# Kernel optimization log

Measured on AMD Instinct MI355X. Metric: run time of the kernel, lower is better.

The kernel has to match this reference:

```python
import jax, jax.numpy as jnp
import numpy as np

B, L, LC, C, H = 4, 1024, 1024, 1024, 16
HD = C // H
SCALE = 0.25 / (HD ** 0.5)
EPS = 1e-5

def _ln(x):
    mu = jnp.mean(x, axis=-1, keepdims=True)
    var = jnp.mean(jnp.square(x - mu), axis=-1, keepdims=True)
    return (x - mu) * jax.lax.rsqrt(var + EPS)

def setup_inputs() -> dict:
    key = jax.random.key(0)
    ks = jax.random.split(key, 16)
    s = 0.02
    return {
        'x': jax.random.normal(ks[0], (B, L, C), jnp.float32),
        'context': jax.random.normal(ks[1], (B, LC, C), jnp.float32),
        'cond_BD': jax.random.normal(ks[2], (B, 1, 6, C), jnp.float32),
        'attn_bias': jax.random.normal(ks[3], (B, H, L, LC), jnp.float32) * 0.1,
        'ada_gss': jax.random.normal(ks[4], (1, 1, 6, C), jnp.float32) / (C ** 0.5),
        'Wq': jax.random.normal(ks[5], (C, C), jnp.float32) * s,
        'Wk': jax.random.normal(ks[6], (C, C), jnp.float32) * s,
        'Wv': jax.random.normal(ks[7], (C, C), jnp.float32) * s,
        'Wo': jax.random.normal(ks[8], (C, C), jnp.float32) * s,
        'bo': jnp.zeros((C,), jnp.float32),
        'W1': jax.random.normal(ks[9], (4 * C, C), jnp.float32) * s,
        'b1': jnp.zeros((4 * C,), jnp.float32),
        'W2': jax.random.normal(ks[10], (C, 4 * C), jnp.float32) * s,
        'b2': jnp.zeros((C,), jnp.float32),
    }

def reference(x, context, cond_BD, attn_bias, ada_gss, Wq, Wk, Wv, Wo, bo, W1, b1, W2, b2):
    # AdaLN params: [B,1,6,C] -> six [B,1,C] tensors
    g = ada_gss + cond_BD
    gamma1, gamma2, scale1, scale2, shift1, shift2 = [g[:, :, i] for i in range(6)]

    # --- cross attention branch ---
    mod_x = _ln(x) * (scale1 + 1.0) + shift1  # [B,L,C]
    q = jnp.einsum('blc,dc->bld', mod_x, Wq).reshape(B, L, H, HD).transpose(0, 2, 1, 3)
    k = jnp.einsum('bmc,dc->bmd', context, Wk).reshape(B, LC, H, HD).transpose(0, 2, 1, 3)
    v = jnp.einsum('bmc,dc->bmd', context, Wv).reshape(B, LC, H, HD).transpose(0, 2, 1, 3)
    attn = jnp.einsum('bhld,bhmd->bhlm', q, k) * SCALE + attn_bias
    attn = jax.nn.softmax(attn, axis=-1)
    out = jnp.einsum('bhlm,bhmd->bhld', attn, v).transpose(0, 2, 1, 3).reshape(B, L, C)
    attn_out = jnp.einsum('blc,dc->bld', out, Wo) + bo
    x = x + attn_out * gamma1

    # --- FFN branch ---
    mod_f = _ln(x) * (scale2 + 1.0) + shift2
    h = jax.nn.gelu(jnp.einsum('blc,hc->blh', mod_f, W1) + b1, approximate=True)
    ffn_out = jnp.einsum('blh,ch->blc', h, W2) + b2
    return x + ffn_out * gamma2
```

## Files before the change

### kernel.cpp

```cpp
#include <hip/hip_runtime.h>

typedef _Float16 half8 __attribute__((ext_vector_type(8)));
typedef _Float16 half4v __attribute__((ext_vector_type(4)));
typedef float f32x4 __attribute__((ext_vector_type(4)));

#define MFMA16(a, b, c) __builtin_amdgcn_mfma_f32_16x16x32_f16((a), (b), (c), 0, 0, 0)

__device__ __forceinline__ void gl2lds16(const void* g, void* l) {
  __builtin_amdgcn_global_load_lds(
      (const __attribute__((address_space(1))) void*)g,
      (__attribute__((address_space(3))) void*)l, 16, 0, 0);
}

__device__ __forceinline__ void cast8(const float* s, _Float16* d, int i) {
  float4 a = *(const float4*)(s + i);
  float4 b = *(const float4*)(s + i + 4);
  half8 o;
  o[0] = (_Float16)a.x; o[1] = (_Float16)a.y; o[2] = (_Float16)a.z; o[3] = (_Float16)a.w;
  o[4] = (_Float16)b.x; o[5] = (_Float16)b.y; o[6] = (_Float16)b.z; o[7] = (_Float16)b.w;
  *(half8*)(d + i) = o;
}

__global__ void cast_all_kernel(const float* s0, const float* s1, const float* s2,
                                const float* s3, const float* s4, const float* s5,
                                const float* s6, _Float16* d0, _Float16* d1,
                                _Float16* d2, _Float16* d3, _Float16* d4,
                                _Float16* d5, _Float16* d6) {
  int b = blockIdx.x;
  const float* s;
  _Float16* d;
  int off;
  if (b < 2048)      { s = s0; d = d0; off = b; }
  else if (b < 2560) { s = s1; d = d1; off = b - 2048; }
  else if (b < 3072) { s = s2; d = d2; off = b - 2560; }
  else if (b < 3584) { s = s3; d = d3; off = b - 3072; }
  else if (b < 4096) { s = s4; d = d4; off = b - 3584; }
  else if (b < 6144) { s = s5; d = d5; off = b - 4096; }
  else               { s = s6; d = d6; off = b - 6144; }
  cast8(s, d, (off * 256 + threadIdx.x) * 8);
}

__global__ void ln_mod_kernel(const float* __restrict__ x, const float* __restrict__ cond,
                              const float* __restrict__ ada, _Float16* __restrict__ out,
                              int sidx, int hidx) {
  int row = blockIdx.x;
  int b = row >> 10;
  int t = threadIdx.x;
  const float* xr = x + (size_t)row * 1024;
  float4 v = *(const float4*)(xr + t * 4);
  float s = v.x + v.y + v.z + v.w;
  float s2 = v.x * v.x + v.y * v.y + v.z * v.z + v.w * v.w;
#pragma unroll
  for (int m = 32; m >= 1; m >>= 1) {
    s += __shfl_xor(s, m, 64);
    s2 += __shfl_xor(s2, m, 64);
  }
  __shared__ float red[8];
  int w = t >> 6;
  if ((t & 63) == 0) { red[w * 2] = s; red[w * 2 + 1] = s2; }
  __syncthreads();
  s = red[0] + red[2] + red[4] + red[6];
  s2 = red[1] + red[3] + red[5] + red[7];
  float mu = s * (1.f / 1024.f);
  float var = s2 * (1.f / 1024.f) - mu * mu;
  float rstd = rsqrtf(var + 1e-5f);
  int c = t * 4;
  float4 sc = *(const float4*)(cond + (size_t)b * 6144 + sidx * 1024 + c);
  float4 sh = *(const float4*)(cond + (size_t)b * 6144 + hidx * 1024 + c);
  float4 sa = *(const float4*)(ada + sidx * 1024 + c);
  float4 ha = *(const float4*)(ada + hidx * 1024 + c);
  half4v o;
  o[0] = (_Float16)((v.x - mu) * rstd * (sc.x + sa.x + 1.f) + sh.x + ha.x);
  o[1] = (_Float16)((v.y - mu) * rstd * (sc.y + sa.y + 1.f) + sh.y + ha.y);
  o[2] = (_Float16)((v.z - mu) * rstd * (sc.z + sa.z + 1.f) + sh.z + ha.z);
  o[3] = (_Float16)((v.w - mu) * rstd * (sc.w + sa.w + 1.f) + sh.w + ha.w);
  *(half4v*)(out + (size_t)row * 1024 + c) = o;
}

template <int EPI>
__global__ __launch_bounds__(256) void gemm_f16(
    const _Float16* __restrict__ A, const _Float16* __restrict__ W,
    int M, int N, int K, void* __restrict__ outp,
    const float* __restrict__ bias, const float* __restrict__ res,
    const float* __restrict__ cond, const float* __restrict__ ada, int gidx) {
  __shared__ __align__(16) _Float16 lA[128 * 32];
  __shared__ __align__(16) _Float16 lB[128 * 32];
  int t = threadIdx.x;
  int lane = t & 63;
  int w = t >> 6;
  int wr = w >> 1, wc = w & 1;
  int l16 = lane & 15, lg = lane >> 4;
  int bm = blockIdx.y * 128, bn = blockIdx.x * 128;
  f32x4 acc[4][4] = {};
  int e0 = t * 8;
  int e1 = 2048 + t * 8;
  int r0 = e0 >> 5, c0 = e0 & 31;
  int r1 = e1 >> 5, c1 = e1 & 31;
  const _Float16* Ab = A + (size_t)bm * K;
  const _Float16* Wb = W + (size_t)bn * K;
  for (int kt = 0; kt < K; kt += 32) {
    gl2lds16(Ab + (size_t)r0 * K + kt + c0, &lA[e0]);
    gl2lds16(Ab + (size_t)r1 * K + kt + c1, &lA[e1]);
    gl2lds16(Wb + (size_t)r0 * K + kt + c0, &lB[e0]);
    gl2lds16(Wb + (size_t)r1 * K + kt + c1, &lB[e1]);
    __syncthreads();
    half8 af[4], bf[4];
#pragma unroll
    for (int m = 0; m < 4; ++m)
      af[m] = *(const half8*)&lA[(wr * 64 + m * 16 + l16) * 32 + lg * 8];
#pragma unroll
    for (int n = 0; n < 4; ++n)
      bf[n] = *(const half8*)&lB[(wc * 64 + n * 16 + l16) * 32 + lg * 8];
#pragma unroll
    for (int m = 0; m < 4; ++m)
#pragma unroll
      for (int n = 0; n < 4; ++n)
        acc[m][n] = MFMA16(af[m], bf[n], acc[m][n]);
    __syncthreads();
  }
#pragma unroll
  for (int m = 0; m < 4; ++m) {
#pragma unroll
    for (int n = 0; n < 4; ++n) {
      int gc = bn + wc * 64 + n * 16 + l16;
      int gr0 = bm + wr * 64 + m * 16 + lg * 4;
#pragma unroll
      for (int r = 0; r < 4; ++r) {
        int gr = gr0 + r;
        float v = acc[m][n][r];
        if constexpr (EPI == 0) {
          int b = gr >> 10, l = gr & 1023, h = gc >> 6, hd = gc & 63;
          ((_Float16*)outp)[(((size_t)(b * 16 + h)) * 1024 + l) * 64 + hd] = (_Float16)v;
        } else if constexpr (EPI == 1) {
          float g = ada[gidx * 1024 + gc] + cond[(size_t)(gr >> 10) * 6144 + gidx * 1024 + gc];
          ((float*)outp)[(size_t)gr * 1024 + gc] =
              res[(size_t)gr * 1024 + gc] + (v + bias[gc]) * g;
        } else {
          float xx = v + bias[gc];
          float u = 0.7978845608028654f * (xx + 0.044715f * xx * xx * xx);
          float e = __expf(2.f * u);
          float th = (e - 1.f) / (e + 1.f);
          ((_Float16*)outp)[(size_t)gr * 4096 + gc] = (_Float16)(0.5f * xx * (1.f + th));
        }
      }
    }
  }
}

__global__ void transpose_v_kernel(const _Float16* __restrict__ v16, _Float16* __restrict__ vt16) {
  int bh = blockIdx.y, ktile = blockIdx.x;
  __shared__ _Float16 tile[64][72];
  int t = threadIdx.x;
  int r = t >> 2, c0 = (t & 3) * 16;
  const _Float16* src = v16 + ((size_t)bh * 1024 + ktile * 64) * 64;
  half8 a = *(const half8*)(src + r * 64 + c0);
  half8 b = *(const half8*)(src + r * 64 + c0 + 8);
#pragma unroll
  for (int j = 0; j < 8; ++j) {
    tile[r][c0 + j] = a[j];
    tile[r][c0 + 8 + j] = b[j];
  }
  __syncthreads();
  half8 oa, ob;
#pragma unroll
  for (int j = 0; j < 8; ++j) {
    oa[j] = tile[c0 + j][r];
    ob[j] = tile[c0 + 8 + j][r];
  }
  _Float16* dst = vt16 + ((size_t)bh * 64 + r) * 1024 + ktile * 64 + c0;
  *(half8*)dst = oa;
  *(half8*)(dst + 8) = ob;
}

__global__ __launch_bounds__(256, 4) void attn_kernel(
    const _Float16* __restrict__ q16, const _Float16* __restrict__ k16,
    const _Float16* __restrict__ vt16, const float* __restrict__ bias,
    _Float16* __restrict__ o16) {
  int bh = blockIdx.y;
  int qb = blockIdx.x;
  int t = threadIdx.x, w = t >> 6, lane = t & 63;
  int l16 = lane & 15, lg = lane >> 4;
  int qRowW = qb * 64 + w * 16;
  const size_t bhoff = (size_t)bh * 65536;
  half8 aq[2];
#pragma unroll
  for (int ks = 0; ks < 2; ++ks)
    aq[ks] = *(const half8*)(q16 + bhoff + (size_t)(qRowW + l16) * 64 + ks * 32 + lg * 8);
  f32x4 oacc[4] = {};
  float mrun = -1e30f, lrun = 0.f;
  __shared__ __align__(16) _Float16 pbuf[4][16][80];
  const float* bb = bias + (size_t)bh * 1048576 + (size_t)(qRowW + l16) * 1024;
  const _Float16* kb = k16 + bhoff;
  const _Float16* vb = vt16 + bhoff;
  f32x4 nb[4];
#pragma unroll
  for (int kk = 0; kk < 4; ++kk) nb[kk] = *(const f32x4*)(bb + kk * 16 + lg * 4);
  for (int kt = 0; kt < 1024; kt += 64) {
    f32x4 s[4] = {};
#pragma unroll
    for (int ks = 0; ks < 2; ++ks) {
#pragma unroll
      for (int kk = 0; kk < 4; ++kk) {
        half8 kf = *(const half8*)(kb + (size_t)(kt + kk * 16 + l16) * 64 + ks * 32 + lg * 8);
        s[kk] = MFMA16(kf, aq[ks], s[kk]);
      }
    }
    float p[4][4];
    float tm = -1e30f;
#pragma unroll
    for (int kk = 0; kk < 4; ++kk)
#pragma unroll
      for (int r = 0; r < 4; ++r) {
        p[kk][r] = s[kk][r] * 0.03125f + nb[kk][r];
        tm = fmaxf(tm, p[kk][r]);
      }
    if (kt < 960) {
#pragma unroll
      for (int kk = 0; kk < 4; ++kk)
        nb[kk] = *(const f32x4*)(bb + kt + 64 + kk * 16 + lg * 4);
    }
    tm = fmaxf(tm, __shfl_xor(tm, 16, 64));
    tm = fmaxf(tm, __shfl_xor(tm, 32, 64));
    int noskip = !__all(tm <= mrun);
    float mnew = noskip ? fmaxf(mrun, tm) : mrun;
    float ts = 0.f;
#pragma unroll
    for (int kk = 0; kk < 4; ++kk)
#pragma unroll
      for (int r = 0; r < 4; ++r) {
        p[kk][r] = exp2f((p[kk][r] - mnew) * 1.442695041f);
        ts += p[kk][r];
      }
    ts += __shfl_xor(ts, 16, 64);
    ts += __shfl_xor(ts, 32, 64);
    if (noskip) {
      float scl = exp2f((mrun - mnew) * 1.442695041f);
      lrun = lrun * scl + ts;
      mrun = mnew;
      float sclr[4];
#pragma unroll
      for (int r = 0; r < 4; ++r) sclr[r] = __shfl(scl, lg * 4 + r, 16);
#pragma unroll
      for (int n = 0; n < 4; ++n)
#pragma unroll
        for (int r = 0; r < 4; ++r) oacc[n][r] *= sclr[r];
    } else {
      lrun += ts;
    }
#pragma unroll
    for (int kk = 0; kk < 4; ++kk) {
      half4v ph;
#pragma unroll
      for (int r = 0; r < 4; ++r) ph[r] = (_Float16)p[kk][r];
      *(half4v*)&pbuf[w][l16][kk * 16 + lg * 4] = ph;
    }
#pragma unroll
    for (int ks = 0; ks < 2; ++ks) {
      half8 ap = *(const half8*)&pbuf[w][l16][ks * 32 + lg * 8];
#pragma unroll
      for (int n = 0; n < 4; ++n) {
        half8 bv = *(const half8*)(vb + (size_t)(n * 16 + l16) * 1024 + kt + ks * 32 + lg * 8);
        oacc[n] = MFMA16(ap, bv, oacc[n]);
      }
    }
  }
  float inv = 1.f / lrun;
  float invr[4];
#pragma unroll
  for (int r = 0; r < 4; ++r) invr[r] = __shfl(inv, lg * 4 + r, 16);
  int b = bh >> 4, h = bh & 15;
#pragma unroll
  for (int r = 0; r < 4; ++r) {
    int row = qRowW + lg * 4 + r;
#pragma unroll
    for (int n = 0; n < 4; ++n)
      o16[((size_t)b * 1024 + row) * 1024 + h * 64 + n * 16 + l16] =
          (_Float16)(oacc[n][r] * invr[r]);
  }
}

extern "C" void kernel_launch(void* const* d_in, const int* in_sizes, int n_in,
                              void* d_out, int out_size, void* d_ws, size_t ws_size,
                              hipStream_t stream) {
  const float* x = (const float*)d_in[0];
  const float* ctx = (const float*)d_in[1];
  const float* cond = (const float*)d_in[2];
  const float* bias = (const float*)d_in[3];
  const float* ada = (const float*)d_in[4];
  const float* Wq = (const float*)d_in[5];
  const float* Wk = (const float*)d_in[6];
  const float* Wv = (const float*)d_in[7];
  const float* Wo = (const float*)d_in[8];
  const float* bo = (const float*)d_in[9];
  const float* W1 = (const float*)d_in[10];
  const float* b1 = (const float*)d_in[11];
  const float* W2 = (const float*)d_in[12];
  const float* b2 = (const float*)d_in[13];

  char* ws = (char*)d_ws;
  const size_t MB = 1u << 20;
  _Float16* wq16 = (_Float16*)(ws + 0 * MB);
  _Float16* wk16 = (_Float16*)(ws + 2 * MB);
  _Float16* wv16 = (_Float16*)(ws + 4 * MB);
  _Float16* wo16 = (_Float16*)(ws + 6 * MB);
  _Float16* w116 = (_Float16*)(ws + 8 * MB);
  _Float16* w216 = (_Float16*)(ws + 16 * MB);
  _Float16* modx = (_Float16*)(ws + 24 * MB);
  _Float16* ctx16 = (_Float16*)(ws + 32 * MB);
  _Float16* q16 = (_Float16*)(ws + 40 * MB);
  _Float16* k16 = (_Float16*)(ws + 48 * MB);
  _Float16* v16 = (_Float16*)(ws + 56 * MB);
  _Float16* vt16 = (_Float16*)(ws + 64 * MB);
  _Float16* h16 = (_Float16*)(ws + 40 * MB);
  _Float16* o16 = (_Float16*)(ws + 72 * MB);
  float* x1 = (float*)(ws + 80 * MB);

  cast_all_kernel<<<8192, 256, 0, stream>>>(ctx, Wq, Wk, Wv, Wo, W1, W2,
                                            ctx16, wq16, wk16, wv16, wo16, w116, w216);

  ln_mod_kernel<<<4096, 256, 0, stream>>>(x, cond, ada, modx, 2, 4);

  dim3 gN1024(8, 32);
  gemm_f16<0><<<gN1024, 256, 0, stream>>>(modx, wq16, 4096, 1024, 1024, q16,
                                          nullptr, nullptr, nullptr, nullptr, 0);
  gemm_f16<0><<<gN1024, 256, 0, stream>>>(ctx16, wk16, 4096, 1024, 1024, k16,
                                          nullptr, nullptr, nullptr, nullptr, 0);
  gemm_f16<0><<<gN1024, 256, 0, stream>>>(ctx16, wv16, 4096, 1024, 1024, v16,
                                          nullptr, nullptr, nullptr, nullptr, 0);

  transpose_v_kernel<<<dim3(16, 64), 256, 0, stream>>>(v16, vt16);

  attn_kernel<<<dim3(16, 64), 256, 0, stream>>>(q16, k16, vt16, bias, o16);

  gemm_f16<1><<<gN1024, 256, 0, stream>>>(o16, wo16, 4096, 1024, 1024, x1,
                                          bo, x, cond, ada, 0);

  ln_mod_kernel<<<4096, 256, 0, stream>>>(x1, cond, ada, modx, 3, 5);

  gemm_f16<2><<<dim3(32, 32), 256, 0, stream>>>(modx, w116, 4096, 4096, 1024, h16,
                                                b1, nullptr, nullptr, nullptr, 0);

  gemm_f16<1><<<gN1024, 256, 0, stream>>>(h16, w216, 4096, 1024, 4096, d_out,
                                          b2, x1, cond, ada, 1);
}
```

Before: 849.5 us.

## Batch QKV GEMMs with transposed V epilogue and split-K attention with LDS bias

Folds the three Q/K/V projection GEMMs into one launch, with a z-dimension selecting the weight, and writes V directly in transposed layout, which removes the separate transpose kernel and its round trip through memory. The attention kernel is restructured so each block handles 16 query rows, with its four waves splitting the key range. Each block stages its 64KB bias tile into LDS with a swizzled async load, and the partial softmax states are merged through LDS at the end. Block IDs are remapped for locality, and the P buffer is XOR-swizzled to avoid bank conflicts. The large LDS footprint lowers occupancy, and the final merge adds extra LDS traffic.

After: 797.7 us. 6.1% less time.

```diff
diff --git a/kernel.cpp b/kernel.cpp
--- a/kernel.cpp
+++ b/kernel.cpp
@@ -75,6 +75,76 @@
   o[2] = (_Float16)((v.z - mu) * rstd * (sc.z + sa.z + 1.f) + sh.z + ha.z);
   o[3] = (_Float16)((v.w - mu) * rstd * (sc.w + sa.w + 1.f) + sh.w + ha.w);
   *(half4v*)(out + (size_t)row * 1024 + c) = o;
+}
+
+__global__ __launch_bounds__(256) void gemm_qkv(
+    const _Float16* __restrict__ modx, const _Float16* __restrict__ ctx16,
+    const _Float16* __restrict__ wq, const _Float16* __restrict__ wk,
+    const _Float16* __restrict__ wv, _Float16* __restrict__ q16,
+    _Float16* __restrict__ k16, _Float16* __restrict__ vt16) {
+  int z = blockIdx.z;
+  const _Float16* A = (z == 0) ? modx : ctx16;
+  const _Float16* W = (z == 0) ? wq : ((z == 1) ? wk : wv);
+  const int K = 1024;
+  __shared__ __align__(16) _Float16 lA[128 * 32];
+  __shared__ __align__(16) _Float16 lB[128 * 32];
+  int t = threadIdx.x;
+  int lane = t & 63;
+  int w = t >> 6;
+  int wr = w >> 1, wc = w & 1;
+  int l16 = lane & 15, lg = lane >> 4;
+  int bm = blockIdx.y * 128, bn = blockIdx.x * 128;
+  f32x4 acc[4][4] = {};
+  int e0 = t * 8;
+  int e1 = 2048 + t * 8;
+  int r0 = e0 >> 5, c0 = e0 & 31;
+  int r1 = e1 >> 5, c1 = e1 & 31;
+  const _Float16* Ab = A + (size_t)bm * K;
+  const _Float16* Wb = W + (size_t)bn * K;
+  for (int kt = 0; kt < K; kt += 32) {
+    gl2lds16(Ab + (size_t)r0 * K + kt + c0, &lA[e0]);
+    gl2lds16(Ab + (size_t)r1 * K + kt + c1, &lA[e1]);
+    gl2lds16(Wb + (size_t)r0 * K + kt + c0, &lB[e0]);
+    gl2lds16(Wb + (size_t)r1 * K + kt + c1, &lB[e1]);
+    __syncthreads();
+    half8 af[4], bf[4];
+#pragma unroll
+    for (int m = 0; m < 4; ++m)
+      af[m] = *(const half8*)&lA[(wr * 64 + m * 16 + l16) * 32 + lg * 8];
+#pragma unroll
+    for (int n = 0; n < 4; ++n)
+      bf[n] = *(const half8*)&lB[(wc * 64 + n * 16 + l16) * 32 + lg * 8];
+#pragma unroll
+    for (int m = 0; m < 4; ++m)
+#pragma unroll
+      for (int n = 0; n < 4; ++n)
+        acc[m][n] = MFMA16(af[m], bf[n], acc[m][n]);
+    __syncthreads();
+  }
+#pragma unroll
+  for (int m = 0; m < 4; ++m) {
+#pragma unroll
+    for (int n = 0; n < 4; ++n) {
+      int gc = bn + wc * 64 + n * 16 + l16;
+      int gr0 = bm + wr * 64 + m * 16 + lg * 4;
+      int h = gc >> 6, hd = gc & 63;
+      if (z < 2) {
+        _Float16* dst = (z == 0) ? q16 : k16;
+#pragma unroll
+        for (int r = 0; r < 4; ++r) {
+          int gr = gr0 + r;
+          int b = gr >> 10, l = gr & 1023;
+          dst[(((size_t)(b * 16 + h)) * 1024 + l) * 64 + hd] = (_Float16)acc[m][n][r];
+        }
+      } else {
+        int b = gr0 >> 10, l = gr0 & 1023;
+        half4v hv;
+#pragma unroll
+        for (int r = 0; r < 4; ++r) hv[r] = (_Float16)acc[m][n][r];
+        *(half4v*)&vt16[(((size_t)(b * 16 + h)) * 64 + hd) * 1024 + l] = hv;
+      }
+    }
+  }
 }
 
 template <int EPI>
@@ -128,10 +198,7 @@
       for (int r = 0; r < 4; ++r) {
         int gr = gr0 + r;
         float v = acc[m][n][r];
-        if constexpr (EPI == 0) {
-          int b = gr >> 10, l = gr & 1023, h = gc >> 6, hd = gc & 63;
-          ((_Float16*)outp)[(((size_t)(b * 16 + h)) * 1024 + l) * 64 + hd] = (_Float16)v;
-        } else if constexpr (EPI == 1) {
+        if constexpr (EPI == 1) {
           float g = ada[gidx * 1024 + gc] + cond[(size_t)(gr >> 10) * 6144 + gidx * 1024 + gc];
           ((float*)outp)[(size_t)gr * 1024 + gc] =
               res[(size_t)gr * 1024 + gc] + (v + bias[gc]) * g;
@@ -147,55 +214,49 @@
   }
 }
 
-__global__ void transpose_v_kernel(const _Float16* __restrict__ v16, _Float16* __restrict__ vt16) {
-  int bh = blockIdx.y, ktile = blockIdx.x;
-  __shared__ _Float16 tile[64][72];
-  int t = threadIdx.x;
-  int r = t >> 2, c0 = (t & 3) * 16;
-  const _Float16* src = v16 + ((size_t)bh * 1024 + ktile * 64) * 64;
-  half8 a = *(const half8*)(src + r * 64 + c0);
-  half8 b = *(const half8*)(src + r * 64 + c0 + 8);
-#pragma unroll
-  for (int j = 0; j < 8; ++j) {
-    tile[r][c0 + j] = a[j];
-    tile[r][c0 + 8 + j] = b[j];
-  }
-  __syncthreads();
-  half8 oa, ob;
-#pragma unroll
-  for (int j = 0; j < 8; ++j) {
-    oa[j] = tile[c0 + j][r];
-    ob[j] = tile[c0 + 8 + j][r];
-  }
-  _Float16* dst = vt16 + ((size_t)bh * 64 + r) * 1024 + ktile * 64 + c0;
-  *(half8*)dst = oa;
-  *(half8*)(dst + 8) = ob;
-}
-
-__global__ __launch_bounds__(256, 4) void attn_kernel(
+__global__ __launch_bounds__(256, 2) void attn_kernel(
     const _Float16* __restrict__ q16, const _Float16* __restrict__ k16,
     const _Float16* __restrict__ vt16, const float* __restrict__ bias,
     _Float16* __restrict__ o16) {
-  int bh = blockIdx.y;
-  int qb = blockIdx.x;
+  int wg = blockIdx.x;
+  int sid = (wg & 7) * 512 + (wg >> 3);
+  int bh = sid >> 6, qb = sid & 63;
   int t = threadIdx.x, w = t >> 6, lane = t & 63;
   int l16 = lane & 15, lg = lane >> 4;
-  int qRowW = qb * 64 + w * 16;
+  int qRow = qb * 16;
+
+  __shared__ __align__(16) char smem[65536 + 8192 + 512];
+  float* biasL = (float*)smem;
+  _Float16* pbuf = (_Float16*)(smem + 65536);
+  float* sm = (float*)(smem + 65536 + 8192);
+  float* sl = sm + 64;
+  float* soL = (float*)smem;
+
+  const char* bsrc = (const char*)(bias + (size_t)bh * 1048576 + (size_t)qRow * 1024);
+#pragma unroll
+  for (int i = 0; i < 16; ++i) {
+    int c = w * 16 + i;
+    int S = c * 64 + lane;
+    int r = S >> 8, s = S & 255;
+    int ss = s ^ (r & 7);
+    gl2lds16(bsrc + (size_t)r * 4096 + (ss << 4), (char*)smem + c * 1024);
+  }
+
   const size_t bhoff = (size_t)bh * 65536;
   half8 aq[2];
 #pragma unroll
   for (int ks = 0; ks < 2; ++ks)
-    aq[ks] = *(const half8*)(q16 + bhoff + (size_t)(qRowW + l16) * 64 + ks * 32 + lg * 8);
+    aq[ks] = *(const half8*)(q16 + bhoff + (size_t)(qRow + l16) * 64 + ks * 32 + lg * 8);
+  const _Float16* kb = k16 + bhoff;
+  const _Float16* vb = vt16 + bhoff;
+
   f32x4 oacc[4] = {};
   float mrun = -1e30f, lrun = 0.f;
-  __shared__ __align__(16) _Float16 pbuf[4][16][80];
-  const float* bb = bias + (size_t)bh * 1048576 + (size_t)(qRowW + l16) * 1024;
-  const _Float16* kb = k16 + bhoff;
-  const _Float16* vb = vt16 + bhoff;
-  f32x4 nb[4];
-#pragma unroll
-  for (int kk = 0; kk < 4; ++kk) nb[kk] = *(const f32x4*)(bb + kk * 16 + lg * 4);
-  for (int kt = 0; kt < 1024; kt += 64) {
+  __syncthreads();
+
+  int ktw = w * 256;
+  for (int it = 0; it < 4; ++it) {
+    int kt = ktw + it * 64;
     f32x4 s[4] = {};
 #pragma unroll
     for (int ks = 0; ks < 2; ++ks) {
@@ -208,16 +269,14 @@
     float p[4][4];
     float tm = -1e30f;
 #pragma unroll
-    for (int kk = 0; kk < 4; ++kk)
+    for (int kk = 0; kk < 4; ++kk) {
+      int slot = (kt >> 2) + 4 * kk + lg;
+      f32x4 bv = *(const f32x4*)(biasL + l16 * 1024 + ((slot ^ (l16 & 7)) << 2));
 #pragma unroll
       for (int r = 0; r < 4; ++r) {
-        p[kk][r] = s[kk][r] * 0.03125f + nb[kk][r];
+        p[kk][r] = s[kk][r] * 0.03125f + bv[r];
         tm = fmaxf(tm, p[kk][r]);
       }
-    if (kt < 960) {
-#pragma unroll
-      for (int kk = 0; kk < 4; ++kk)
-        nb[kk] = *(const f32x4*)(bb + kt + 64 + kk * 16 + lg * 4);
     }
     tm = fmaxf(tm, __shfl_xor(tm, 16, 64));
     tm = fmaxf(tm, __shfl_xor(tm, 32, 64));
@@ -247,16 +306,18 @@
     } else {
       lrun += ts;
     }
+    char* pb = (char*)pbuf + w * 2048 + l16 * 128;
 #pragma unroll
     for (int kk = 0; kk < 4; ++kk) {
       half4v ph;
 #pragma unroll
       for (int r = 0; r < 4; ++r) ph[r] = (_Float16)p[kk][r];
-      *(half4v*)&pbuf[w][l16][kk * 16 + lg * 4] = ph;
+      int slot = 2 * kk + (lg >> 1);
+      *(half4v*)(pb + ((slot ^ (l16 & 7)) << 4) + (lg & 1) * 8) = ph;
     }
 #pragma unroll
     for (int ks = 0; ks < 2; ++ks) {
-      half8 ap = *(const half8*)&pbuf[w][l16][ks * 32 + lg * 8];
+      half8 ap = *(const half8*)(pb + (((4 * ks + lg) ^ (l16 & 7)) << 4));
 #pragma unroll
       for (int n = 0; n < 4; ++n) {
         half8 bv = *(const half8*)(vb + (size_t)(n * 16 + l16) * 1024 + kt + ks * 32 + lg * 8);
@@ -264,19 +325,34 @@
       }
     }
   }
-  float inv = 1.f / lrun;
-  float invr[4];
-#pragma unroll
-  for (int r = 0; r < 4; ++r) invr[r] = __shfl(inv, lg * 4 + r, 16);
+
+  __syncthreads();
+  if (lg == 0) { sm[w * 16 + l16] = mrun; sl[w * 16 + l16] = lrun; }
+#pragma unroll
+  for (int n = 0; n < 4; ++n)
+#pragma unroll
+    for (int r = 0; r < 4; ++r)
+      soL[(size_t)(w * 16 + lg * 4 + r) * 68 + n * 16 + l16] = oacc[n][r];
+  __syncthreads();
+
+  int q = t >> 4, hq = t & 15;
+  float m0 = sm[q], m1 = sm[16 + q], m2 = sm[32 + q], m3 = sm[48 + q];
+  float M = fmaxf(fmaxf(m0, m1), fmaxf(m2, m3));
+  float e0 = exp2f((m0 - M) * 1.442695041f);
+  float e1 = exp2f((m1 - M) * 1.442695041f);
+  float e2 = exp2f((m2 - M) * 1.442695041f);
+  float e3 = exp2f((m3 - M) * 1.442695041f);
+  float rd = 1.f / (e0 * sl[q] + e1 * sl[16 + q] + e2 * sl[32 + q] + e3 * sl[48 + q]);
   int b = bh >> 4, h = bh & 15;
-#pragma unroll
-  for (int r = 0; r < 4; ++r) {
-    int row = qRowW + lg * 4 + r;
-#pragma unroll
-    for (int n = 0; n < 4; ++n)
-      o16[((size_t)b * 1024 + row) * 1024 + h * 64 + n * 16 + l16] =
-          (_Float16)(oacc[n][r] * invr[r]);
-  }
+  half4v ov;
+#pragma unroll
+  for (int j = 0; j < 4; ++j) {
+    int hd = hq * 4 + j;
+    float num = e0 * soL[(size_t)q * 68 + hd] + e1 * soL[(size_t)(16 + q) * 68 + hd] +
+                e2 * soL[(size_t)(32 + q) * 68 + hd] + e3 * soL[(size_t)(48 + q) * 68 + hd];
+    ov[j] = (_Float16)(num * rd);
+  }
+  *(half4v*)&o16[((size_t)b * 1024 + qRow + q) * 1024 + h * 64 + hq * 4] = ov;
 }
 
 extern "C" void kernel_launch(void* const* d_in, const int* in_sizes, int n_in,
@@ -309,7 +385,6 @@
   _Float16* ctx16 = (_Float16*)(ws + 32 * MB);
   _Float16* q16 = (_Float16*)(ws + 40 * MB);
   _Float16* k16 = (_Float16*)(ws + 48 * MB);
-  _Float16* v16 = (_Float16*)(ws + 56 * MB);
   _Float16* vt16 = (_Float16*)(ws + 64 * MB);
   _Float16* h16 = (_Float16*)(ws + 40 * MB);
   _Float16* o16 = (_Float16*)(ws + 72 * MB);
@@ -320,18 +395,12 @@
 
   ln_mod_kernel<<<4096, 256, 0, stream>>>(x, cond, ada, modx, 2, 4);
 
+  gemm_qkv<<<dim3(8, 32, 3), 256, 0, stream>>>(modx, ctx16, wq16, wk16, wv16,
+                                               q16, k16, vt16);
+
+  attn_kernel<<<4096, 256, 0, stream>>>(q16, k16, vt16, bias, o16);
+
   dim3 gN1024(8, 32);
-  gemm_f16<0><<<gN1024, 256, 0, stream>>>(modx, wq16, 4096, 1024, 1024, q16,
-                                          nullptr, nullptr, nullptr, nullptr, 0);
-  gemm_f16<0><<<gN1024, 256, 0, stream>>>(ctx16, wk16, 4096, 1024, 1024, k16,
-                                          nullptr, nullptr, nullptr, nullptr, 0);
-  gemm_f16<0><<<gN1024, 256, 0, stream>>>(ctx16, wv16, 4096, 1024, 1024, v16,
-                                          nullptr, nullptr, nullptr, nullptr, 0);
-
-  transpose_v_kernel<<<dim3(16, 64), 256, 0, stream>>>(v16, vt16);
-
-  attn_kernel<<<dim3(16, 64), 256, 0, stream>>>(q16, k16, vt16, bias, o16);
-
   gemm_f16<1><<<gN1024, 256, 0, stream>>>(o16, wo16, 4096, 1024, 1024, x1,
                                           bo, x, cond, ada, 0);
 
```
